# Performance work log

Hardware: AMD Instinct MI355X
Metric: run time of the kernel (lower is better)

The kernel has to match this reference:

```python
import jax, jax.numpy as jnp
import numpy as np

N, E, F, H = 100000, 1000000, 128, 64
BN_EPS = 1e-3  # keras BatchNormalization default epsilon


def setup_inputs() -> dict:
    key = jax.random.key(0)
    k_x, k_src, k_dst, k_w = jax.random.split(key, 4)
    node_features = jax.random.normal(k_x, (N, F), dtype=jnp.float32)
    # Ensure every node appears at least once as a source so that
    # deg**-0.5 is finite (the original code implicitly assumes this).
    src = jnp.concatenate([
        jnp.arange(N, dtype=jnp.int32),
        jax.random.randint(k_src, (E - N,), 0, N, dtype=jnp.int32),
    ])
    dst = jax.random.randint(k_dst, (E,), 0, N, dtype=jnp.int32)
    edge_index = jnp.stack([src, dst], axis=1)  # [E, 2]
    # glorot_uniform for kernel
    limit = np.sqrt(6.0 / (F + H)).astype(np.float32)
    W = jax.random.uniform(k_w, (F, H), dtype=jnp.float32, minval=-limit, maxval=limit)
    b = jnp.zeros((H,), dtype=jnp.float32)
    bn_gamma = jnp.ones((H,), dtype=jnp.float32)
    bn_beta = jnp.zeros((H,), dtype=jnp.float32)
    bn_mean = jnp.zeros((H,), dtype=jnp.float32)
    bn_var = jnp.ones((H,), dtype=jnp.float32)
    return dict(node_features=node_features, W=W, b=b, bn_gamma=bn_gamma,
                bn_beta=bn_beta, bn_mean=bn_mean, bn_var=bn_var,
                edge_index=edge_index)


def reference(node_features, W, b, bn_gamma, bn_beta, bn_mean, bn_var, edge_index):
    n = node_features.shape[0]
    src = edge_index[:, 0]
    dst = edge_index[:, 1]
    # Dense transform; dropout is identity in inference (training=False).
    h = node_features @ W + b  # [N, H]
    # Out-degree per node (segments keyed by src, matching the TF code).
    deg = jax.ops.segment_sum(jnp.ones(src.shape, h.dtype), src, num_segments=n)  # [N]
    inv_sqrt_deg = deg ** -0.5
    # Per-edge symmetric-style scaling: deg(src)^-0.5 * deg(dst)^-0.5 * h[dst]
    edge_scale = inv_sqrt_deg[src] * inv_sqrt_deg[dst]  # [E]
    neigh = edge_scale[:, None] * h[dst]  # [E, H]
    agg = 0.5 * jax.ops.segment_sum(neigh, src, num_segments=n)  # [N, H]
    # Self term: segment_mean of deg(src) * h[src] over src segments.
    self_term = deg[src][:, None] * h[src]  # [E, H]
    self_sum = jax.ops.segment_sum(self_term, src, num_segments=n)  # [N, H]
    self_mean = self_sum / jnp.maximum(deg, 1.0)[:, None]
    agg = agg + 0.5 * self_mean
    # BatchNormalization in inference mode.
    out = (agg - bn_mean) * (bn_gamma * jax.lax.rsqrt(bn_var + BN_EPS)) + bn_beta
    return out
```

## Files before the change

kernel.cpp:

```cpp
#include <hip/hip_runtime.h>

#define BN_EPS 0.001f
#define CAP 32

typedef __attribute__((ext_vector_type(8))) short bf16x8;
typedef __attribute__((ext_vector_type(4))) float f32x4;

__device__ __forceinline__ unsigned short f2bf(float f) {
  unsigned u = __float_as_uint(f);
  u += 0x7fffu + ((u >> 16) & 1u);
  return (unsigned short)(u >> 16);
}
__device__ __forceinline__ unsigned scale2(unsigned u, float s) {
  float lo = __uint_as_float(u << 16) * s;
  float hi = __uint_as_float(u & 0xffff0000u) * s;
  return (((unsigned)f2bf(hi)) << 16) | (unsigned)f2bf(lo);
}

__global__ __launch_bounds__(256) void k_fused(
    const float* __restrict__ X, const float* __restrict__ W,
    const float* __restrict__ B, unsigned short* __restrict__ hb, int N, int Gg,
    const int2* __restrict__ ei, int* __restrict__ cnt,
    int* __restrict__ ell, int E, int Gs) {
  __shared__ float WtF[4096];

  int g = blockIdx.x / 7;
  int r = blockIdx.x % 7;
  int tid = threadIdx.x;

  if (r >= 2) {
    int chunk = g * 5 + (r - 2);
    if (chunk >= Gs) return;
    int e = chunk * 256 + tid;
    if (e < E) {
      int2 sd = ei[e];
      int pos = atomicAdd(&cnt[sd.x], 1);
      if (pos < CAP) ell[(size_t)sd.x * CAP + pos] = sd.y;
    }
    return;
  }

  int tile = g * 2 + r;
  if (tile >= Gg) return;

  char* Wt = (char*)WtF;
  const float4* W4 = (const float4*)W;
  for (int i = tid; i < 2048; i += 256) {
    float4 v = W4[i];
    int k = i >> 4;
    int col0 = (i & 15) << 2;
    int kb2 = k << 1;
    *(unsigned short*)(Wt + (((col0 + 0) << 8) | (kb2 ^ (((col0 + 0) & 7) << 4)))) = f2bf(v.x);
    *(unsigned short*)(Wt + (((col0 + 1) << 8) | (kb2 ^ (((col0 + 1) & 7) << 4)))) = f2bf(v.y);
    *(unsigned short*)(Wt + (((col0 + 2) << 8) | (kb2 ^ (((col0 + 2) & 7) << 4)))) = f2bf(v.z);
    *(unsigned short*)(Wt + (((col0 + 3) << 8) | (kb2 ^ (((col0 + 3) & 7) << 4)))) = f2bf(v.w);
  }
  __syncthreads();

  int lane = tid & 63;
  int w = tid >> 6;
  int l15 = lane & 15;
  int lk = lane >> 4;

  int row0 = tile * 64;
  int rA = row0 + w * 16 + l15;
  bool rowok = rA < N;
  const float* xp = X + (size_t)rA * 128 + (lk << 3);

  f32x4 acc[4];
  #pragma unroll
  for (int n = 0; n < 4; ++n) {
    float bv = B[(n << 4) + l15];
    acc[n] = (f32x4){bv, bv, bv, bv};
  }

  #pragma unroll
  for (int kb = 0; kb < 4; ++kb) {
    bf16x8 af = {0, 0, 0, 0, 0, 0, 0, 0};
    if (rowok) {
      float4 x0 = *(const float4*)(xp + kb * 32);
      float4 x1 = *(const float4*)(xp + kb * 32 + 4);
      af[0] = (short)f2bf(x0.x); af[1] = (short)f2bf(x0.y);
      af[2] = (short)f2bf(x0.z); af[3] = (short)f2bf(x0.w);
      af[4] = (short)f2bf(x1.x); af[5] = (short)f2bf(x1.y);
      af[6] = (short)f2bf(x1.z); af[7] = (short)f2bf(x1.w);
    }
    int kbyte = (kb << 6) | (lk << 4);
    #pragma unroll
    for (int n = 0; n < 4; ++n) {
      int col = (n << 4) + l15;
      bf16x8 bfr = *(const bf16x8*)(Wt + ((col << 8) | (kbyte ^ ((col & 7) << 4))));
      acc[n] = __builtin_amdgcn_mfma_f32_16x16x32_bf16(af, bfr, acc[n], 0, 0, 0);
    }
  }

  int rbase = row0 + w * 16 + (lk << 2);
  #pragma unroll
  for (int n = 0; n < 4; ++n) {
    #pragma unroll
    for (int q = 0; q < 4; ++q) {
      int row = rbase + q;
      if (row < N) hb[(size_t)row * 64 + (n << 4) + l15] = f2bf(acc[n][q]);
    }
  }
}

__global__ __launch_bounds__(256) void k_scale(const unsigned int* __restrict__ hb32,
                                               const int* __restrict__ cnt,
                                               unsigned int* __restrict__ hbs32, int N) {
  int t = blockIdx.x * 256 + threadIdx.x;
  int node = t >> 3;
  int q = t & 7;
  if (node >= N) return;
  int c = cnt[node];
  float s = rsqrtf((float)((c > 0) ? c : 1));
  uint4 v = ((const uint4*)(hb32 + (size_t)node * 32))[q];
  v.x = scale2(v.x, s); v.y = scale2(v.y, s);
  v.z = scale2(v.z, s); v.w = scale2(v.w, s);
  ((uint4*)(hbs32 + (size_t)node * 32))[q] = v;
}

__global__ __launch_bounds__(256) void k_aggfinal_s(const int* __restrict__ cnt,
                                                    const int* __restrict__ ell,
                                                    const unsigned int* __restrict__ hb32,
                                                    const unsigned int* __restrict__ hbs32,
                                                    const float* __restrict__ gamma,
                                                    const float* __restrict__ beta,
                                                    const float* __restrict__ mean,
                                                    const float* __restrict__ var,
                                                    float* __restrict__ out, int N) {
  int wave = threadIdx.x >> 6;
  int lane = threadIdx.x & 63;
  int sub  = lane >> 5;
  int fp   = lane & 31;
  int node = blockIdx.x * 8 + wave * 2 + sub;
  if (node >= N) return;

  int d_raw = ell[(size_t)node * CAP + fp];
  int c0 = cnt[node];
  unsigned us = hb32[(size_t)node * 32 + fp];
  int dm = ((unsigned)d_raw < (unsigned)N) ? d_raw : 0;
  int c = (c0 < CAP) ? c0 : CAP;
  int base = sub << 5;

  float ax = 0.f, ay = 0.f;
  int q = 0;
  for (; q + 8 <= c; q += 8) {
    int d[8];
    #pragma unroll
    for (int i = 0; i < 8; ++i) d[i] = __shfl(dm, base + q + i);
    unsigned u[8];
    #pragma unroll
    for (int i = 0; i < 8; ++i) u[i] = hbs32[(size_t)d[i] * 32 + fp];
    #pragma unroll
    for (int i = 0; i < 8; ++i) {
      ax += __uint_as_float(u[i] << 16);
      ay += __uint_as_float(u[i] & 0xffff0000u);
    }
  }
  if (q + 4 <= c) {
    int d0 = __shfl(dm, base + q);
    int d1 = __shfl(dm, base + q + 1);
    int d2 = __shfl(dm, base + q + 2);
    int d3 = __shfl(dm, base + q + 3);
    unsigned u0 = hbs32[(size_t)d0 * 32 + fp];
    unsigned u1 = hbs32[(size_t)d1 * 32 + fp];
    unsigned u2 = hbs32[(size_t)d2 * 32 + fp];
    unsigned u3 = hbs32[(size_t)d3 * 32 + fp];
    ax += __uint_as_float(u0 << 16);
    ay += __uint_as_float(u0 & 0xffff0000u);
    ax += __uint_as_float(u1 << 16);
    ay += __uint_as_float(u1 & 0xffff0000u);
    ax += __uint_as_float(u2 << 16);
    ay += __uint_as_float(u2 & 0xffff0000u);
    ax += __uint_as_float(u3 << 16);
    ay += __uint_as_float(u3 & 0xffff0000u);
    q += 4;
  }
  for (; q < c; ++q) {
    int dq = __shfl(dm, base + q);
    unsigned u = hbs32[(size_t)dq * 32 + fp];
    ax += __uint_as_float(u << 16);
    ay += __uint_as_float(u & 0xffff0000u);
  }

  int j = fp * 2;
  float hx = __uint_as_float(us << 16);
  float hy = __uint_as_float(us & 0xffff0000u);

  float degf = (float)c0;
  float isd_n = rsqrtf((float)((c0 > 0) ? c0 : 1));
  float rx = 0.5f * (isd_n * ax + degf * hx);
  float ry = 0.5f * (isd_n * ay + degf * hy);

  float2 gm = *(const float2*)&gamma[j];
  float2 bt = *(const float2*)&beta[j];
  float2 mn = *(const float2*)&mean[j];
  float2 vr = *(const float2*)&var[j];
  float2 o;
  o.x = (rx - mn.x) * (gm.x * rsqrtf(vr.x + BN_EPS)) + bt.x;
  o.y = (ry - mn.y) * (gm.y * rsqrtf(vr.y + BN_EPS)) + bt.y;
  *(float2*)&out[(size_t)node * 64 + j] = o;
}

__global__ __launch_bounds__(256) void k_aggfinal_g(const int* __restrict__ cnt,
                                                    const int* __restrict__ ell,
                                                    const unsigned int* __restrict__ hb32,
                                                    const float* __restrict__ gamma,
                                                    const float* __restrict__ beta,
                                                    const float* __restrict__ mean,
                                                    const float* __restrict__ var,
                                                    float* __restrict__ out, int N) {
  int wave = threadIdx.x >> 6;
  int lane = threadIdx.x & 63;
  int sub  = lane >> 5;
  int fp   = lane & 31;
  int node = blockIdx.x * 8 + wave * 2 + sub;
  if (node >= N) return;

  int d_raw = ell[(size_t)node * CAP + fp];
  int c0 = cnt[node];
  int dm = ((unsigned)d_raw < (unsigned)N) ? d_raw : 0;
  int c = (c0 < CAP) ? c0 : CAP;
  float s = 0.f;
  if (fp < c) s = rsqrtf((float)cnt[dm]);
  int base = sub << 5;

  float ax = 0.f, ay = 0.f;
  int q = 0;
  for (; q + 4 <= c; q += 4) {
    int d0 = __shfl(dm, base + q);
    int d1 = __shfl(dm, base + q + 1);
    int d2 = __shfl(dm, base + q + 2);
    int d3 = __shfl(dm, base + q + 3);
    float s0 = __shfl(s, base + q);
    float s1 = __shfl(s, base + q + 1);
    float s2 = __shfl(s, base + q + 2);
    float s3 = __shfl(s, base + q + 3);
    unsigned u0 = hb32[(size_t)d0 * 32 + fp];
    unsigned u1 = hb32[(size_t)d1 * 32 + fp];
    unsigned u2 = hb32[(size_t)d2 * 32 + fp];
    unsigned u3 = hb32[(size_t)d3 * 32 + fp];
    ax = fmaf(s0, __uint_as_float(u0 << 16), ax);
    ay = fmaf(s0, __uint_as_float(u0 & 0xffff0000u), ay);
    ax = fmaf(s1, __uint_as_float(u1 << 16), ax);
    ay = fmaf(s1, __uint_as_float(u1 & 0xffff0000u), ay);
    ax = fmaf(s2, __uint_as_float(u2 << 16), ax);
    ay = fmaf(s2, __uint_as_float(u2 & 0xffff0000u), ay);
    ax = fmaf(s3, __uint_as_float(u3 << 16), ax);
    ay = fmaf(s3, __uint_as_float(u3 & 0xffff0000u), ay);
  }
  for (; q < c; ++q) {
    int dq = __shfl(dm, base + q);
    float sq = __shfl(s, base + q);
    unsigned u = hb32[(size_t)dq * 32 + fp];
    ax = fmaf(sq, __uint_as_float(u << 16), ax);
    ay = fmaf(sq, __uint_as_float(u & 0xffff0000u), ay);
  }

  int j = fp * 2;
  unsigned us = hb32[(size_t)node * 32 + fp];
  float hx = __uint_as_float(us << 16);
  float hy = __uint_as_float(us & 0xffff0000u);

  float degf = (float)c0;
  float isd_n = rsqrtf((float)((c0 > 0) ? c0 : 1));
  float rx = 0.5f * (isd_n * ax + degf * hx);
  float ry = 0.5f * (isd_n * ay + degf * hy);

  float2 gm = *(const float2*)&gamma[j];
  float2 bt = *(const float2*)&beta[j];
  float2 mn = *(const float2*)&mean[j];
  float2 vr = *(const float2*)&var[j];
  float2 o;
  o.x = (rx - mn.x) * (gm.x * rsqrtf(vr.x + BN_EPS)) + bt.x;
  o.y = (ry - mn.y) * (gm.y * rsqrtf(vr.y + BN_EPS)) + bt.y;
  *(float2*)&out[(size_t)node * 64 + j] = o;
}

extern "C" void kernel_launch(void* const* d_in, const int* in_sizes, int n_in,
                              void* d_out, int out_size, void* d_ws, size_t ws_size,
                              hipStream_t stream) {
  const float* X     = (const float*)d_in[0];
  const float* W     = (const float*)d_in[1];
  const float* B     = (const float*)d_in[2];
  const float* gamma = (const float*)d_in[3];
  const float* beta  = (const float*)d_in[4];
  const float* mean  = (const float*)d_in[5];
  const float* var   = (const float*)d_in[6];
  const int2*  ei    = (const int2*)d_in[7];

  int N = in_sizes[0] / 128;
  int E = in_sizes[7] / 2;
  float* out = (float*)d_out;

  size_t hb_elems = (size_t)N * 64;
  size_t need_hbs = hb_elems * 2 * 2 + (size_t)N * CAP * 4 + (size_t)N * 4;

  int Gs = (E + 255) / 256;
  int Gg = (N + 63) / 64;
  int g7 = (Gg + 1) / 2;
  int g5 = (Gs + 4) / 5;
  int groups = (g7 > g5) ? g7 : g5;

  if (ws_size >= need_hbs) {
    unsigned short* hb  = (unsigned short*)d_ws;
    unsigned short* hbs = hb + hb_elems;
    int*            ell = (int*)(hbs + hb_elems);
    int*            cnt = ell + (size_t)N * CAP;

    hipMemsetAsync(cnt, 0, (size_t)N * sizeof(int), stream);
    k_fused<<<groups * 7, 256, 0, stream>>>(X, W, B, hb, N, Gg, ei, cnt, ell, E, Gs);
    k_scale<<<(N * 8 + 255) / 256, 256, 0, stream>>>((const unsigned int*)hb, cnt,
                                                     (unsigned int*)hbs, N);
    k_aggfinal_s<<<(N + 7) / 8, 256, 0, stream>>>(cnt, ell, (const unsigned int*)hb,
                                                  (const unsigned int*)hbs,
                                                  gamma, beta, mean, var, out, N);
  } else {
    unsigned short* hb  = (unsigned short*)d_ws;
    int*            ell = (int*)(hb + hb_elems);
    int*            cnt = ell + (size_t)N * CAP;

    hipMemsetAsync(cnt, 0, (size_t)N * sizeof(int), stream);
    k_fused<<<groups * 7, 256, 0, stream>>>(X, W, B, hb, N, Gg, ei, cnt, ell, E, Gs);
    k_aggfinal_g<<<(N + 7) / 8, 256, 0, stream>>>(cnt, ell, (const unsigned int*)hb,
                                                  gamma, beta, mean, var, out, N);
  }
}
```

Measured before the change: 200.6 us.

## Transpose ELL adjacency to slot-major and stage neighbor lists in LDS

The edge scatter now writes the capped neighbor list in slot-major order (pos*N+src) instead of node-major. The aggregation kernel handles 64 nodes per block: it loads the transposed neighbor lists into shared memory with coalesced reads, then each half-wave walks 8 nodes in turn, reading indices from LDS instead of using lane shuffles. The goal is cheaper, coalesced index fetches and fewer shuffles. The cost is less parallelism per node, since nodes are processed sequentially within a half-wave, plus extra LDS traffic and a sync; the scatter writes also become strided across N.

```diff
diff --git a/kernel.cpp b/kernel.cpp
--- a/kernel.cpp
+++ b/kernel.cpp
@@ -21,7 +21,7 @@
     const float* __restrict__ X, const float* __restrict__ W,
     const float* __restrict__ B, unsigned short* __restrict__ hb, int N, int Gg,
     const int2* __restrict__ ei, int* __restrict__ cnt,
-    int* __restrict__ ell, int E, int Gs) {
+    int* __restrict__ ell_t, int E, int Gs) {
   __shared__ float WtF[4096];
 
   int g = blockIdx.x / 7;
@@ -35,7 +35,7 @@
     if (e < E) {
       int2 sd = ei[e];
       int pos = atomicAdd(&cnt[sd.x], 1);
-      if (pos < CAP) ell[(size_t)sd.x * CAP + pos] = sd.y;
+      if (pos < CAP) ell_t[(size_t)pos * N + sd.x] = sd.y;
     }
     return;
   }
@@ -120,162 +120,200 @@
   ((uint4*)(hbs32 + (size_t)node * 32))[q] = v;
 }
 
-__global__ __launch_bounds__(256) void k_aggfinal_s(const int* __restrict__ cnt,
-                                                    const int* __restrict__ ell,
-                                                    const unsigned int* __restrict__ hb32,
-                                                    const unsigned int* __restrict__ hbs32,
-                                                    const float* __restrict__ gamma,
-                                                    const float* __restrict__ beta,
-                                                    const float* __restrict__ mean,
-                                                    const float* __restrict__ var,
-                                                    float* __restrict__ out, int N) {
-  int wave = threadIdx.x >> 6;
-  int lane = threadIdx.x & 63;
-  int sub  = lane >> 5;
-  int fp   = lane & 31;
-  int node = blockIdx.x * 8 + wave * 2 + sub;
-  if (node >= N) return;
-
-  int d_raw = ell[(size_t)node * CAP + fp];
-  int c0 = cnt[node];
-  unsigned us = hb32[(size_t)node * 32 + fp];
-  int dm = ((unsigned)d_raw < (unsigned)N) ? d_raw : 0;
-  int c = (c0 < CAP) ? c0 : CAP;
-  int base = sub << 5;
-
-  float ax = 0.f, ay = 0.f;
-  int q = 0;
-  for (; q + 8 <= c; q += 8) {
-    int d[8];
-    #pragma unroll
-    for (int i = 0; i < 8; ++i) d[i] = __shfl(dm, base + q + i);
-    unsigned u[8];
-    #pragma unroll
-    for (int i = 0; i < 8; ++i) u[i] = hbs32[(size_t)d[i] * 32 + fp];
-    #pragma unroll
-    for (int i = 0; i < 8; ++i) {
-      ax += __uint_as_float(u[i] << 16);
-      ay += __uint_as_float(u[i] & 0xffff0000u);
-    }
-  }
-  if (q + 4 <= c) {
-    int d0 = __shfl(dm, base + q);
-    int d1 = __shfl(dm, base + q + 1);
-    int d2 = __shfl(dm, base + q + 2);
-    int d3 = __shfl(dm, base + q + 3);
-    unsigned u0 = hbs32[(size_t)d0 * 32 + fp];
-    unsigned u1 = hbs32[(size_t)d1 * 32 + fp];
-    unsigned u2 = hbs32[(size_t)d2 * 32 + fp];
-    unsigned u3 = hbs32[(size_t)d3 * 32 + fp];
-    ax += __uint_as_float(u0 << 16);
-    ay += __uint_as_float(u0 & 0xffff0000u);
-    ax += __uint_as_float(u1 << 16);
-    ay += __uint_as_float(u1 & 0xffff0000u);
-    ax += __uint_as_float(u2 << 16);
-    ay += __uint_as_float(u2 & 0xffff0000u);
-    ax += __uint_as_float(u3 << 16);
-    ay += __uint_as_float(u3 & 0xffff0000u);
-    q += 4;
-  }
-  for (; q < c; ++q) {
-    int dq = __shfl(dm, base + q);
-    unsigned u = hbs32[(size_t)dq * 32 + fp];
-    ax += __uint_as_float(u << 16);
-    ay += __uint_as_float(u & 0xffff0000u);
-  }
-
-  int j = fp * 2;
-  float hx = __uint_as_float(us << 16);
-  float hy = __uint_as_float(us & 0xffff0000u);
-
-  float degf = (float)c0;
-  float isd_n = rsqrtf((float)((c0 > 0) ? c0 : 1));
-  float rx = 0.5f * (isd_n * ax + degf * hx);
-  float ry = 0.5f * (isd_n * ay + degf * hy);
-
-  float2 gm = *(const float2*)&gamma[j];
-  float2 bt = *(const float2*)&beta[j];
-  float2 mn = *(const float2*)&mean[j];
-  float2 vr = *(const float2*)&var[j];
-  float2 o;
-  o.x = (rx - mn.x) * (gm.x * rsqrtf(vr.x + BN_EPS)) + bt.x;
-  o.y = (ry - mn.y) * (gm.y * rsqrtf(vr.y + BN_EPS)) + bt.y;
-  *(float2*)&out[(size_t)node * 64 + j] = o;
-}
-
-__global__ __launch_bounds__(256) void k_aggfinal_g(const int* __restrict__ cnt,
-                                                    const int* __restrict__ ell,
-                                                    const unsigned int* __restrict__ hb32,
-                                                    const float* __restrict__ gamma,
-                                                    const float* __restrict__ beta,
-                                                    const float* __restrict__ mean,
-                                                    const float* __restrict__ var,
-                                                    float* __restrict__ out, int N) {
-  int wave = threadIdx.x >> 6;
-  int lane = threadIdx.x & 63;
-  int sub  = lane >> 5;
-  int fp   = lane & 31;
-  int node = blockIdx.x * 8 + wave * 2 + sub;
-  if (node >= N) return;
-
-  int d_raw = ell[(size_t)node * CAP + fp];
-  int c0 = cnt[node];
-  int dm = ((unsigned)d_raw < (unsigned)N) ? d_raw : 0;
-  int c = (c0 < CAP) ? c0 : CAP;
-  float s = 0.f;
-  if (fp < c) s = rsqrtf((float)cnt[dm]);
-  int base = sub << 5;
-
-  float ax = 0.f, ay = 0.f;
-  int q = 0;
-  for (; q + 4 <= c; q += 4) {
-    int d0 = __shfl(dm, base + q);
-    int d1 = __shfl(dm, base + q + 1);
-    int d2 = __shfl(dm, base + q + 2);
-    int d3 = __shfl(dm, base + q + 3);
-    float s0 = __shfl(s, base + q);
-    float s1 = __shfl(s, base + q + 1);
-    float s2 = __shfl(s, base + q + 2);
-    float s3 = __shfl(s, base + q + 3);
-    unsigned u0 = hb32[(size_t)d0 * 32 + fp];
-    unsigned u1 = hb32[(size_t)d1 * 32 + fp];
-    unsigned u2 = hb32[(size_t)d2 * 32 + fp];
-    unsigned u3 = hb32[(size_t)d3 * 32 + fp];
-    ax = fmaf(s0, __uint_as_float(u0 << 16), ax);
-    ay = fmaf(s0, __uint_as_float(u0 & 0xffff0000u), ay);
-    ax = fmaf(s1, __uint_as_float(u1 << 16), ax);
-    ay = fmaf(s1, __uint_as_float(u1 & 0xffff0000u), ay);
-    ax = fmaf(s2, __uint_as_float(u2 << 16), ax);
-    ay = fmaf(s2, __uint_as_float(u2 & 0xffff0000u), ay);
-    ax = fmaf(s3, __uint_as_float(u3 << 16), ax);
-    ay = fmaf(s3, __uint_as_float(u3 & 0xffff0000u), ay);
-  }
-  for (; q < c; ++q) {
-    int dq = __shfl(dm, base + q);
-    float sq = __shfl(s, base + q);
-    unsigned u = hb32[(size_t)dq * 32 + fp];
-    ax = fmaf(sq, __uint_as_float(u << 16), ax);
-    ay = fmaf(sq, __uint_as_float(u & 0xffff0000u), ay);
-  }
-
-  int j = fp * 2;
-  unsigned us = hb32[(size_t)node * 32 + fp];
-  float hx = __uint_as_float(us << 16);
-  float hy = __uint_as_float(us & 0xffff0000u);
-
-  float degf = (float)c0;
-  float isd_n = rsqrtf((float)((c0 > 0) ? c0 : 1));
-  float rx = 0.5f * (isd_n * ax + degf * hx);
-  float ry = 0.5f * (isd_n * ay + degf * hy);
-
-  float2 gm = *(const float2*)&gamma[j];
-  float2 bt = *(const float2*)&beta[j];
-  float2 mn = *(const float2*)&mean[j];
-  float2 vr = *(const float2*)&var[j];
-  float2 o;
-  o.x = (rx - mn.x) * (gm.x * rsqrtf(vr.x + BN_EPS)) + bt.x;
-  o.y = (ry - mn.y) * (gm.y * rsqrtf(vr.y + BN_EPS)) + bt.y;
-  *(float2*)&out[(size_t)node * 64 + j] = o;
+__global__ __launch_bounds__(256) void k_agg2(const int* __restrict__ cnt,
+                                              const int* __restrict__ ell_t,
+                                              const unsigned int* __restrict__ hb32,
+                                              const unsigned int* __restrict__ hbs32,
+                                              const float* __restrict__ gamma,
+                                              const float* __restrict__ beta,
+                                              const float* __restrict__ mean,
+                                              const float* __restrict__ var,
+                                              float* __restrict__ out, int N) {
+  __shared__ int lds_dst[CAP * 64];
+  __shared__ int lds_cnt[64];
+
+  int tid = threadIdx.x;
+  int node0 = blockIdx.x * 64;
+
+  if (tid < 64) {
+    int n = node0 + tid;
+    lds_cnt[tid] = (n < N) ? cnt[n] : 0;
+  }
+  for (int i = tid; i < CAP * 64; i += 256) {
+    int j = i & 63;
+    int p = i >> 6;
+    int n = node0 + j;
+    lds_dst[i] = (n < N) ? ell_t[(size_t)p * N + n] : 0;
+  }
+  __syncthreads();
+
+  int hw = tid >> 5;
+  int fp = tid & 31;
+
+  float2 gm = *(const float2*)&gamma[fp * 2];
+  float2 bt = *(const float2*)&beta[fp * 2];
+  float2 mn = *(const float2*)&mean[fp * 2];
+  float2 vr = *(const float2*)&var[fp * 2];
+  float gsx = gm.x * rsqrtf(vr.x + BN_EPS);
+  float gsy = gm.y * rsqrtf(vr.y + BN_EPS);
+
+  #pragma unroll
+  for (int t = 0; t < 8; ++t) {
+    int j = hw * 8 + t;
+    int node = node0 + j;
+    if (node >= N) continue;
+    int c0 = lds_cnt[j];
+    int c = (c0 < CAP) ? c0 : CAP;
+    unsigned us = hb32[(size_t)node * 32 + fp];
+
+    float ax = 0.f, ay = 0.f;
+    int q = 0;
+    for (; q + 8 <= c; q += 8) {
+      int d[8];
+      #pragma unroll
+      for (int i = 0; i < 8; ++i) {
+        int dr = lds_dst[(q + i) * 64 + j];
+        d[i] = ((unsigned)dr < (unsigned)N) ? dr : 0;
+      }
+      unsigned u[8];
+      #pragma unroll
+      for (int i = 0; i < 8; ++i) u[i] = hbs32[(size_t)d[i] * 32 + fp];
+      #pragma unroll
+      for (int i = 0; i < 8; ++i) {
+        ax += __uint_as_float(u[i] << 16);
+        ay += __uint_as_float(u[i] & 0xffff0000u);
+      }
+    }
+    if (q + 4 <= c) {
+      int d0 = lds_dst[(q + 0) * 64 + j]; d0 = ((unsigned)d0 < (unsigned)N) ? d0 : 0;
+      int d1 = lds_dst[(q + 1) * 64 + j]; d1 = ((unsigned)d1 < (unsigned)N) ? d1 : 0;
+      int d2 = lds_dst[(q + 2) * 64 + j]; d2 = ((unsigned)d2 < (unsigned)N) ? d2 : 0;
+      int d3 = lds_dst[(q + 3) * 64 + j]; d3 = ((unsigned)d3 < (unsigned)N) ? d3 : 0;
+      unsigned u0 = hbs32[(size_t)d0 * 32 + fp];
+      unsigned u1 = hbs32[(size_t)d1 * 32 + fp];
+      unsigned u2 = hbs32[(size_t)d2 * 32 + fp];
+      unsigned u3 = hbs32[(size_t)d3 * 32 + fp];
+      ax += __uint_as_float(u0 << 16);
+      ay += __uint_as_float(u0 & 0xffff0000u);
+      ax += __uint_as_float(u1 << 16);
+      ay += __uint_as_float(u1 & 0xffff0000u);
+      ax += __uint_as_float(u2 << 16);
+      ay += __uint_as_float(u2 & 0xffff0000u);
+      ax += __uint_as_float(u3 << 16);
+      ay += __uint_as_float(u3 & 0xffff0000u);
+      q += 4;
+    }
+    for (; q < c; ++q) {
+      int dq = lds_dst[q * 64 + j];
+      dq = ((unsigned)dq < (unsigned)N) ? dq : 0;
+      unsigned u = hbs32[(size_t)dq * 32 + fp];
+      ax += __uint_as_float(u << 16);
+      ay += __uint_as_float(u & 0xffff0000u);
+    }
+
+    float hx = __uint_as_float(us << 16);
+    float hy = __uint_as_float(us & 0xffff0000u);
+    float degf = (float)c0;
+    float isd_n = rsqrtf((float)((c0 > 0) ? c0 : 1));
+    float rx = 0.5f * (isd_n * ax + degf * hx);
+    float ry = 0.5f * (isd_n * ay + degf * hy);
+
+    float2 o;
+    o.x = (rx - mn.x) * gsx + bt.x;
+    o.y = (ry - mn.y) * gsy + bt.y;
+    *(float2*)&out[(size_t)node * 64 + fp * 2] = o;
+  }
+}
+
+__global__ __launch_bounds__(256) void k_agg2_g(const int* __restrict__ cnt,
+                                                const int* __restrict__ ell_t,
+                                                const unsigned int* __restrict__ hb32,
+                                                const float* __restrict__ gamma,
+                                                const float* __restrict__ beta,
+                                                const float* __restrict__ mean,
+                                                const float* __restrict__ var,
+                                                float* __restrict__ out, int N) {
+  __shared__ int lds_dst[CAP * 64];
+  __shared__ int lds_cnt[64];
+
+  int tid = threadIdx.x;
+  int node0 = blockIdx.x * 64;
+
+  if (tid < 64) {
+    int n = node0 + tid;
+    lds_cnt[tid] = (n < N) ? cnt[n] : 0;
+  }
+  for (int i = tid; i < CAP * 64; i += 256) {
+    int j = i & 63;
+    int p = i >> 6;
+    int n = node0 + j;
+    lds_dst[i] = (n < N) ? ell_t[(size_t)p * N + n] : 0;
+  }
+  __syncthreads();
+
+  int hw = tid >> 5;
+  int fp = tid & 31;
+
+  float2 gm = *(const float2*)&gamma[fp * 2];
+  float2 bt = *(const float2*)&beta[fp * 2];
+  float2 mn = *(const float2*)&mean[fp * 2];
+  float2 vr = *(const float2*)&var[fp * 2];
+  float gsx = gm.x * rsqrtf(vr.x + BN_EPS);
+  float gsy = gm.y * rsqrtf(vr.y + BN_EPS);
+
+  for (int t = 0; t < 8; ++t) {
+    int j = hw * 8 + t;
+    int node = node0 + j;
+    if (node >= N) continue;
+    int c0 = lds_cnt[j];
+    int c = (c0 < CAP) ? c0 : CAP;
+    unsigned us = hb32[(size_t)node * 32 + fp];
+
+    float ax = 0.f, ay = 0.f;
+    int q = 0;
+    for (; q + 4 <= c; q += 4) {
+      int d0 = lds_dst[(q + 0) * 64 + j]; d0 = ((unsigned)d0 < (unsigned)N) ? d0 : 0;
+      int d1 = lds_dst[(q + 1) * 64 + j]; d1 = ((unsigned)d1 < (unsigned)N) ? d1 : 0;
+      int d2 = lds_dst[(q + 2) * 64 + j]; d2 = ((unsigned)d2 < (unsigned)N) ? d2 : 0;
+      int d3 = lds_dst[(q + 3) * 64 + j]; d3 = ((unsigned)d3 < (unsigned)N) ? d3 : 0;
+      float s0 = rsqrtf((float)max(cnt[d0], 1));
+      float s1 = rsqrtf((float)max(cnt[d1], 1));
+      float s2 = rsqrtf((float)max(cnt[d2], 1));
+      float s3 = rsqrtf((float)max(cnt[d3], 1));
+      unsigned u0 = hb32[(size_t)d0 * 32 + fp];
+      unsigned u1 = hb32[(size_t)d1 * 32 + fp];
+      unsigned u2 = hb32[(size_t)d2 * 32 + fp];
+      unsigned u3 = hb32[(size_t)d3 * 32 + fp];
+      ax = fmaf(s0, __uint_as_float(u0 << 16), ax);
+      ay = fmaf(s0, __uint_as_float(u0 & 0xffff0000u), ay);
+      ax = fmaf(s1, __uint_as_float(u1 << 16), ax);
+      ay = fmaf(s1, __uint_as_float(u1 & 0xffff0000u), ay);
+      ax = fmaf(s2, __uint_as_float(u2 << 16), ax);
+      ay = fmaf(s2, __uint_as_float(u2 & 0xffff0000u), ay);
+      ax = fmaf(s3, __uint_as_float(u3 << 16), ax);
+      ay = fmaf(s3, __uint_as_float(u3 & 0xffff0000u), ay);
+    }
+    for (; q < c; ++q) {
+      int dq = lds_dst[q * 64 + j];
+      dq = ((unsigned)dq < (unsigned)N) ? dq : 0;
+      float sq = rsqrtf((float)max(cnt[dq], 1));
+      unsigned u = hb32[(size_t)dq * 32 + fp];
+      ax = fmaf(sq, __uint_as_float(u << 16), ax);
+      ay = fmaf(sq, __uint_as_float(u & 0xffff0000u), ay);
+    }
+
+    float hx = __uint_as_float(us << 16);
+    float hy = __uint_as_float(us & 0xffff0000u);
+    float degf = (float)c0;
+    float isd_n = rsqrtf((float)((c0 > 0) ? c0 : 1));
+    float rx = 0.5f * (isd_n * ax + degf * hx);
+    float ry = 0.5f * (isd_n * ay + degf * hy);
+
+    float2 o;
+    o.x = (rx - mn.x) * gsx + bt.x;
+    o.y = (ry - mn.y) * gsy + bt.y;
+    *(float2*)&out[(size_t)node * 64 + fp * 2] = o;
+  }
 }
 
 extern "C" void kernel_launch(void* const* d_in, const int* in_sizes, int n_in,
@@ -302,6 +340,7 @@
   int g7 = (Gg + 1) / 2;
   int g5 = (Gs + 4) / 5;
   int groups = (g7 > g5) ? g7 : g5;
+  int Ga = (N + 63) / 64;
 
   if (ws_size >= need_hbs) {
     unsigned short* hb  = (unsigned short*)d_ws;
@@ -313,9 +352,9 @@
     k_fused<<<groups * 7, 256, 0, stream>>>(X, W, B, hb, N, Gg, ei, cnt, ell, E, Gs);
     k_scale<<<(N * 8 + 255) / 256, 256, 0, stream>>>((const unsigned int*)hb, cnt,
                                                      (unsigned int*)hbs, N);
-    k_aggfinal_s<<<(N + 7) / 8, 256, 0, stream>>>(cnt, ell, (const unsigned int*)hb,
-                                                  (const unsigned int*)hbs,
-                                                  gamma, beta, mean, var, out, N);
+    k_agg2<<<Ga, 256, 0, stream>>>(cnt, ell, (const unsigned int*)hb,
+                                   (const unsigned int*)hbs,
+                                   gamma, beta, mean, var, out, N);
   } else {
     unsigned short* hb  = (unsigned short*)d_ws;
     int*            ell = (int*)(hb + hb_elems);
@@ -323,7 +362,7 @@
 
     hipMemsetAsync(cnt, 0, (size_t)N * sizeof(int), stream);
     k_fused<<<groups * 7, 256, 0, stream>>>(X, W, B, hb, N, Gg, ei, cnt, ell, E, Gs);
-    k_aggfinal_g<<<(N + 7) / 8, 256, 0, stream>>>(cnt, ell, (const unsigned int*)hb,
-                                                  gamma, beta, mean, var, out, N);
-  }
-}
+    k_agg2_g<<<Ga, 256, 0, stream>>>(cnt, ell, (const unsigned int*)hb,
+                                     gamma, beta, mean, var, out, N);
+  }
+}
```

Measured after the change: 199.5 us. No clear change (-0.6%).
